# Optimization experiments

Hardware: AMD Instinct MI355X
Metric: run time of the kernel (lower is better)

The kernel has to match this reference:

```python
import jax, jax.numpy as jnp
import numpy as np

B, S, F, H = 64, 2048, 1024, 1024

def setup_inputs() -> dict:
    key = jax.random.key(0)
    ks = jax.random.split(key, 16)
    inp = {
        "input": jax.random.normal(ks[0], (B,), jnp.float32),
        "hidden": jax.random.normal(ks[1], (1, B, H), jnp.float32),
        "encoder_outputs": jax.random.normal(ks[2], (B, S, F), jnp.float32),
        "attention_mask": jax.random.randint(ks[3], (B, S), 0, 2, jnp.int32),
    }
    s = lambda n: 1.0 / np.sqrt(n)
    inp["attn_W"] = jax.random.uniform(ks[4], (1, F + H + 1), jnp.float32, -s(F+H+1), s(F+H+1))
    inp["attn_b"] = jax.random.uniform(ks[5], (1,), jnp.float32, -s(F+H+1), s(F+H+1))
    inp["combine_W"] = jax.random.uniform(ks[6], (H, F + 1), jnp.float32, -s(F+1), s(F+1))
    inp["combine_b"] = jax.random.uniform(ks[7], (H,), jnp.float32, -s(F+1), s(F+1))
    inp["W_ih"] = jax.random.uniform(ks[8], (3 * H, H), jnp.float32, -s(H), s(H))
    inp["W_hh"] = jax.random.uniform(ks[9], (3 * H, H), jnp.float32, -s(H), s(H))
    inp["b_ih"] = jax.random.uniform(ks[10], (3 * H,), jnp.float32, -s(H), s(H))
    inp["b_hh"] = jax.random.uniform(ks[11], (3 * H,), jnp.float32, -s(H), s(H))
    inp["out_W"] = jax.random.uniform(ks[12], (1, H), jnp.float32, -s(H), s(H))
    inp["out_b"] = jax.random.uniform(ks[13], (1,), jnp.float32, -s(H), s(H))
    return inp


def reference(input, hidden, encoder_outputs, attention_mask,
              attn_W, attn_b, combine_W, combine_b,
              W_ih, W_hh, b_ih, b_hh, out_W, out_b):
    # Dropout in eval mode (identity); faithful to deterministic inference.
    h = hidden[0]                                   # [B, H]
    # Additive attention score: Linear over cat(enc, h_expanded, input_expanded)
    # is split into three partial matmuls (same math, no [B,S,F+H+1] concat).
    w_e = attn_W[0, :F]                             # [F]
    w_h = attn_W[0, F:F + H]                        # [H]
    w_i = attn_W[0, -1]                             # scalar
    scores = (jnp.einsum('bsf,f->bs', encoder_outputs, w_e)
              + (h @ w_h)[:, None]
              + input[:, None] * w_i
              + attn_b[0])                          # [B, S]
    scores = jnp.where(attention_mask == 0, jnp.float32(-1e10), scores)
    attn_weights = jax.nn.softmax(scores, axis=1)   # [B, S]
    attn_applied = jnp.einsum('bs,bsf->bf', attn_weights, encoder_outputs)  # [B, F]

    x = jnp.concatenate([input[:, None], attn_applied], axis=1)  # [B, F+1]
    x = jax.nn.relu(x @ combine_W.T + combine_b)    # [B, H]

    # Single GRU step (PyTorch gate order: r, z, n)
    gi = x @ W_ih.T + b_ih                          # [B, 3H]
    gh = h @ W_hh.T + b_hh                          # [B, 3H]
    r = jax.nn.sigmoid(gi[:, :H] + gh[:, :H])
    z = jax.nn.sigmoid(gi[:, H:2 * H] + gh[:, H:2 * H])
    n = jnp.tanh(gi[:, 2 * H:] + r * gh[:, 2 * H:])
    h_new = (1.0 - z) * n + z * h                   # [B, H]

    out = jax.nn.relu(h_new) @ out_W.T + out_b      # [B, 1]
    return out[:, 0], h_new[None], attn_weights[:, :, None]
```

## Files before the change

### kernel.cpp

```cpp
#include <hip/hip_runtime.h>
#include <math.h>

#define BB 64
#define SS 2048
#define FF 1024
#define HH 1024
#define NCHUNK 32
#define KSPLIT 8
#define KCH 128

#define WS_PL    0
#define WS_XT    2048
#define WS_HT    (WS_XT+65536)
#define WS_X2T   (WS_HT+65536)
#define WS_EPART (WS_X2T+65536)
#define WS_GPART (WS_EPART+524288)
#define WS_PACC  (WS_GPART+3145728)

__device__ __forceinline__ float sigm(float x){ return 1.f/(1.f + __expf(-x)); }

__global__ __launch_bounds__(256) void kB(const float* __restrict__ enc,
                                          const int*   __restrict__ mask,
                                          const float* __restrict__ attn_W,
                                          const float* __restrict__ input,
                                          const float* __restrict__ hidden,
                                          const float* __restrict__ attn_b,
                                          float* __restrict__ scores_out,
                                          float* __restrict__ pacc,
                                          float* __restrict__ pl)
{
    const int tid  = threadIdx.x;
    const int lane = tid & 63;
    const int w    = tid >> 6;
    const int b    = blockIdx.x >> 5;
    const int c    = blockIdx.x & 31;
    const int s0   = c*64;

    const float4* we4 = (const float4*)attn_W;
    const float4 we0 = we4[lane], we1 = we4[64+lane], we2 = we4[128+lane], we3 = we4[192+lane];

    const float4* h4  = (const float4*)(hidden + (size_t)b*HH);
    const float4* wh4 = (const float4*)(attn_W + FF);
    float4 hv0 = h4[lane], hv1 = h4[64+lane], hv2 = h4[128+lane], hv3 = h4[192+lane];
    float4 wv0 = wh4[lane], wv1 = wh4[64+lane], wv2 = wh4[128+lane], wv3 = wh4[192+lane];
    float bp = hv0.x*wv0.x + hv0.y*wv0.y + hv0.z*wv0.z + hv0.w*wv0.w
             + hv1.x*wv1.x + hv1.y*wv1.y + hv1.z*wv1.z + hv1.w*wv1.w
             + hv2.x*wv2.x + hv2.y*wv2.y + hv2.z*wv2.z + hv2.w*wv2.w
             + hv3.x*wv3.x + hv3.y*wv3.y + hv3.z*wv3.z + hv3.w*wv3.w;
    #pragma unroll
    for (int off=32; off; off>>=1) bp += __shfl_xor(bp, off);
    const float bb = bp + input[b]*attn_W[FF+HH] + attn_b[0];

    int m = mask[b*SS + s0 + lane];
    unsigned long long v = __ballot(m != 0);
    int cnt = (int)__popcll(v);
    int share = (cnt + 3) >> 2;
    int start = w*share; if (start > cnt) start = cnt;
    int end = start + share; if (end > cnt) end = cnt;
    int mycount = end - start;

    unsigned long long vv = v;
    for (int i=0; i<start; ++i) vv &= vv - 1;

    const float4* encw = (const float4*)(enc + (size_t)(b*SS + s0)*FF);

    float l = 0.f;
    float4 a0 = make_float4(0,0,0,0), a1 = a0, a2 = a0, a3 = a0;
    float sc_keep = 0.f;
    unsigned long long written = 0ull;

    int npair = mycount >> 1;
    for (int p=0; p<npair; ++p){
        int rA = (int)__builtin_ctzll(vv); vv &= vv-1;
        int rB = (int)__builtin_ctzll(vv); vv &= vv-1;
        const float4* pA = encw + (size_t)rA*(FF/4);
        const float4* pB = encw + (size_t)rB*(FF/4);
        float4 e0 = pA[lane], e1 = pA[64+lane], e2 = pA[128+lane], e3 = pA[192+lane];
        float4 f0 = pB[lane], f1 = pB[64+lane], f2 = pB[128+lane], f3 = pB[192+lane];
        float da = (e0.x*we0.x + e0.y*we0.y + e0.z*we0.z + e0.w*we0.w)
                 + (e1.x*we1.x + e1.y*we1.y + e1.z*we1.z + e1.w*we1.w)
                 + (e2.x*we2.x + e2.y*we2.y + e2.z*we2.z + e2.w*we2.w)
                 + (e3.x*we3.x + e3.y*we3.y + e3.z*we3.z + e3.w*we3.w);
        float db = (f0.x*we0.x + f0.y*we0.y + f0.z*we0.z + f0.w*we0.w)
                 + (f1.x*we1.x + f1.y*we1.y + f1.z*we1.z + f1.w*we1.w)
                 + (f2.x*we2.x + f2.y*we2.y + f2.z*we2.z + f2.w*we2.w)
                 + (f3.x*we3.x + f3.y*we3.y + f3.z*we3.z + f3.w*we3.w);
        #pragma unroll
        for (int off=32; off; off>>=1){ da += __shfl_xor(da, off); db += __shfl_xor(db, off); }
        float scA = da + bb, scB = db + bb;
        float pAe = __expf(scA), pBe = __expf(scB);
        l += pAe + pBe;
        a0.x += pAe*e0.x + pBe*f0.x; a0.y += pAe*e0.y + pBe*f0.y; a0.z += pAe*e0.z + pBe*f0.z; a0.w += pAe*e0.w + pBe*f0.w;
        a1.x += pAe*e1.x + pBe*f1.x; a1.y += pAe*e1.y + pBe*f1.y; a1.z += pAe*e1.z + pBe*f1.z; a1.w += pAe*e1.w + pBe*f1.w;
        a2.x += pAe*e2.x + pBe*f2.x; a2.y += pAe*e2.y + pBe*f2.y; a2.z += pAe*e2.z + pBe*f2.z; a2.w += pAe*e2.w + pBe*f2.w;
        a3.x += pAe*e3.x + pBe*f3.x; a3.y += pAe*e3.y + pBe*f3.y; a3.z += pAe*e3.z + pBe*f3.z; a3.w += pAe*e3.w + pBe*f3.w;
        sc_keep = (lane == rA) ? scA : sc_keep;
        sc_keep = (lane == rB) ? scB : sc_keep;
        written |= (1ull << rA) | (1ull << rB);
    }
    if (mycount & 1){
        int rA = (int)__builtin_ctzll(vv);
        const float4* pA = encw + (size_t)rA*(FF/4);
        float4 e0 = pA[lane], e1 = pA[64+lane], e2 = pA[128+lane], e3 = pA[192+lane];
        float da = (e0.x*we0.x + e0.y*we0.y + e0.z*we0.z + e0.w*we0.w)
                 + (e1.x*we1.x + e1.y*we1.y + e1.z*we1.z + e1.w*we1.w)
                 + (e2.x*we2.x + e2.y*we2.y + e2.z*we2.z + e2.w*we2.w)
                 + (e3.x*we3.x + e3.y*we3.y + e3.z*we3.z + e3.w*we3.w);
        #pragma unroll
        for (int off=32; off; off>>=1) da += __shfl_xor(da, off);
        float scA = da + bb;
        float pAe = __expf(scA);
        l += pAe;
        a0.x += pAe*e0.x; a0.y += pAe*e0.y; a0.z += pAe*e0.z; a0.w += pAe*e0.w;
        a1.x += pAe*e1.x; a1.y += pAe*e1.y; a1.z += pAe*e1.z; a1.w += pAe*e1.w;
        a2.x += pAe*e2.x; a2.y += pAe*e2.y; a2.z += pAe*e2.z; a2.w += pAe*e2.w;
        a3.x += pAe*e3.x; a3.y += pAe*e3.y; a3.z += pAe*e3.z; a3.w += pAe*e3.w;
        sc_keep = (lane == rA) ? scA : sc_keep;
        written |= (1ull << rA);
    }
    if ((written >> lane) & 1ull) scores_out[b*SS + s0 + lane] = sc_keep;
    if (w == 0 && m == 0)         scores_out[b*SS + s0 + lane] = -1e10f;

    __shared__ float4 sacc[4][256];
    __shared__ float sl[4];
    if (lane==0) sl[w] = l;
    sacc[w][lane]     = a0;
    sacc[w][64+lane]  = a1;
    sacc[w][128+lane] = a2;
    sacc[w][192+lane] = a3;
    __syncthreads();
    float4 tot = sacc[0][tid];
    #pragma unroll
    for (int q=1;q<4;q++){ float4 u = sacc[q][tid]; tot.x+=u.x; tot.y+=u.y; tot.z+=u.z; tot.w+=u.w; }
    ((float4*)(pacc + (size_t)blockIdx.x*FF))[tid] = tot;
    if (tid==0) pl[blockIdx.x] = sl[0]+sl[1]+sl[2]+sl[3];
}

__global__ __launch_bounds__(256) void kC(const float* __restrict__ pacc,
                                          const float* __restrict__ pl,
                                          const float* __restrict__ hidden,
                                          const float* __restrict__ out_b,
                                          float* __restrict__ xT,
                                          float* __restrict__ wout,
                                          float* __restrict__ hT,
                                          float* __restrict__ out)
{
    int b = blockIdx.x >> 2, q = blockIdx.x & 3, tid = threadIdx.x;
    float L = 0.f;
    #pragma unroll
    for (int c=0;c<NCHUNK;c++) L += pl[b*NCHUNK+c];
    float invL = 1.f/L;

    int f = q*256 + tid;
    float a = 0.f;
    #pragma unroll
    for (int c=0;c<NCHUNK;c++) a += pacc[((size_t)(b*NCHUNK+c))*FF + f];
    xT[(size_t)f*BB + b] = a*invL;

    if (q == 0){
        for (int t = tid; t < SS; t += 256){
            int idx2 = b*SS + t;
            wout[idx2] = __expf(wout[idx2]) * invL;
        }
    } else if (q == 1){
        for (int k = tid; k < HH; k += 256) hT[(size_t)k*BB + b] = hidden[(size_t)b*HH + k];
    } else if (q == 2){
        if (tid == 0) out[b] = out_b[0];
    }
}

__global__ __launch_bounds__(256) void kE1(const float* __restrict__ xT,
                                           const float* __restrict__ cW,
                                           float* __restrict__ epart)
{
    __shared__ __align__(16) float Xl[KCH*64];
    __shared__ __align__(16) float Wl[16*KCH];
    int tid = threadIdx.x, lane = tid&63, w = tid>>6;
    int jb = blockIdx.x >> 3, kc = blockIdx.x & 7;
    int j0 = jb*16, k0 = kc*KCH;

    const float4* xs = (const float4*)(xT + (size_t)k0*BB);
    float4* xd = (float4*)Xl;
    #pragma unroll
    for (int r=tid; r<KCH*16; r+=256) xd[r] = xs[r];
    for (int idx=tid; idx<16*KCH; idx+=256){
        int row = idx>>7, kk = idx&127;
        Wl[idx] = cW[(size_t)(j0+row)*(FF+1) + 1 + k0 + kk];
    }
    __syncthreads();

    float acc[4] = {0.f,0.f,0.f,0.f};
    const float* wp = Wl + (w*4)*KCH;
    for (int kk=0; kk<KCH; kk+=4){
        float x0 = Xl[kk*64+lane], x1 = Xl[(kk+1)*64+lane];
        float x2 = Xl[(kk+2)*64+lane], x3 = Xl[(kk+3)*64+lane];
        #pragma unroll
        for (int jj=0;jj<4;jj++){
            float4 wv = *(const float4*)(wp + jj*KCH + kk);
            acc[jj] += x0*wv.x + x1*wv.y + x2*wv.z + x3*wv.w;
        }
    }
    #pragma unroll
    for (int jj=0;jj<4;jj++)
        epart[((size_t)kc*HH + j0 + w*4 + jj)*BB + lane] = acc[jj];
}

__global__ __launch_bounds__(256) void kE2(const float* __restrict__ epart,
                                           const float* __restrict__ input,
                                           const float* __restrict__ cW,
                                           const float* __restrict__ cb,
                                           float* __restrict__ x2T)
{
    int tid = threadIdx.x, lane = tid&63, w = tid>>6;
    int j = blockIdx.x*4 + w;
    float s = 0.f;
    #pragma unroll
    for (int kc=0;kc<KSPLIT;kc++) s += epart[((size_t)kc*HH + j)*BB + lane];
    s += input[lane]*cW[(size_t)j*(FF+1)] + cb[j];
    x2T[(size_t)j*BB + lane] = fmaxf(s, 0.f);
}

__global__ __launch_bounds__(256) void kF1(const float* __restrict__ x2T,
                                           const float* __restrict__ hT,
                                           const float* __restrict__ W_ih,
                                           const float* __restrict__ W_hh,
                                           float* __restrict__ gpart)
{
    __shared__ __align__(16) float Xl[KCH*64];
    __shared__ __align__(16) float Wl[16*KCH];
    int tid = threadIdx.x, lane = tid&63, w = tid>>6;
    int rb = blockIdx.x >> 3, kc = blockIdx.x & 7;
    int r0 = rb*16, k0 = kc*KCH;
    bool ih = (r0 < 3*HH);
    const float* X  = ih ? x2T : hT;
    const float* Wb = ih ? (W_ih + (size_t)r0*HH) : (W_hh + (size_t)(r0-3*HH)*HH);

    const float4* xs = (const float4*)(X + (size_t)k0*BB);
    float4* xd = (float4*)Xl;
    #pragma unroll
    for (int r=tid; r<KCH*16; r+=256) xd[r] = xs[r];
    float4* wd = (float4*)Wl;
    #pragma unroll
    for (int idx4=tid; idx4<16*KCH/4; idx4+=256){
        int row = idx4>>5, kq = idx4&31;
        wd[idx4] = *(const float4*)(Wb + (size_t)row*HH + k0 + kq*4);
    }
    __syncthreads();

    float acc[4] = {0.f,0.f,0.f,0.f};
    const float* wp = Wl + (w*4)*KCH;
    for (int kk=0; kk<KCH; kk+=4){
        float x0 = Xl[kk*64+lane], x1 = Xl[(kk+1)*64+lane];
        float x2 = Xl[(kk+2)*64+lane], x3 = Xl[(kk+3)*64+lane];
        #pragma unroll
        for (int jj=0;jj<4;jj++){
            float4 wv = *(const float4*)(wp + jj*KCH + kk);
            acc[jj] += x0*wv.x + x1*wv.y + x2*wv.z + x3*wv.w;
        }
    }
    #pragma unroll
    for (int jj=0;jj<4;jj++)
        gpart[((size_t)kc*6*HH + r0 + w*4 + jj)*BB + lane] = acc[jj];
}

__global__ __launch_bounds__(256) void kF2(const float* __restrict__ gpart,
                                           const float* __restrict__ b_ih,
                                           const float* __restrict__ b_hh,
                                           const float* __restrict__ hT,
                                           const float* __restrict__ out_W,
                                           float* __restrict__ hnew,
                                           float* __restrict__ out)
{
    int tid = threadIdx.x, lane = tid&63, w = tid>>6;
    int j = blockIdx.x*4 + w;
    float g[6];
    #pragma unroll
    for (int gi=0; gi<6; gi++){
        int row = (gi < 3) ? (gi*HH + j) : (3*HH + (gi-3)*HH + j);
        float s = 0.f;
        #pragma unroll
        for (int kc=0;kc<KSPLIT;kc++) s += gpart[((size_t)kc*6*HH + row)*BB + lane];
        g[gi] = s;
    }
    float r = sigm(g[0]+b_ih[j]        + g[3]+b_hh[j]);
    float z = sigm(g[1]+b_ih[HH+j]     + g[4]+b_hh[HH+j]);
    float n = tanhf(g[2]+b_ih[2*HH+j]  + r*(g[5]+b_hh[2*HH+j]));
    float hold = hT[(size_t)j*BB + lane];
    float hn = (1.f - z)*n + z*hold;
    hnew[(size_t)lane*HH + j] = hn;
    float pv = fmaxf(hn, 0.f) * out_W[j];
    __shared__ float red[4][64];
    red[w][lane] = pv;
    __syncthreads();
    if (w==0) atomicAdd(out + lane, red[0][lane]+red[1][lane]+red[2][lane]+red[3][lane]);
}

extern "C" void kernel_launch(void* const* d_in, const int* in_sizes, int n_in,
                              void* d_out, int out_size, void* d_ws, size_t ws_size,
                              hipStream_t stream) {
    const float* input     = (const float*)d_in[0];
    const float* hidden    = (const float*)d_in[1];
    const float* enc       = (const float*)d_in[2];
    const int*   mask      = (const int*)  d_in[3];
    const float* attn_W    = (const float*)d_in[4];
    const float* attn_b    = (const float*)d_in[5];
    const float* combine_W = (const float*)d_in[6];
    const float* combine_b = (const float*)d_in[7];
    const float* W_ih      = (const float*)d_in[8];
    const float* W_hh      = (const float*)d_in[9];
    const float* b_ih      = (const float*)d_in[10];
    const float* b_hh      = (const float*)d_in[11];
    const float* out_W     = (const float*)d_in[12];
    const float* out_b     = (const float*)d_in[13];

    float* out  = (float*)d_out;
    float* hnew = out + 64;
    float* attw = out + 64 + BB*HH;
    float* ws   = (float*)d_ws;

    kB <<<BB*NCHUNK, 256, 0, stream>>>(enc, mask, attn_W, input, hidden, attn_b,
                                       attw, ws+WS_PACC, ws+WS_PL);
    kC <<<256,  256, 0, stream>>>(ws+WS_PACC, ws+WS_PL, hidden, out_b,
                                  ws+WS_XT, attw, ws+WS_HT, out);
    kE1<<<512,  256, 0, stream>>>(ws+WS_XT, combine_W, ws+WS_EPART);
    kE2<<<256,  256, 0, stream>>>(ws+WS_EPART, input, combine_W, combine_b, ws+WS_X2T);
    kF1<<<3072, 256, 0, stream>>>(ws+WS_X2T, ws+WS_HT, W_ih, W_hh, ws+WS_GPART);
    kF2<<<256,  256, 0, stream>>>(ws+WS_GPART, b_ih, b_hh, ws+WS_HT, out_W, hnew, out);
}
```

Before: 102.5 us.

## Fold W_hh GEMV into attention kernel and drop hidden transpose staging

The h @ W_hh part of the GRU does not depend on attention, so it moves into extra blocks appended to the attention kernel's grid. It can then overlap with the memory-bound encoder pass instead of running after it in kF1. The hidden transpose in kC goes away; the new blocks read hidden row-wise and kF2 reads it directly. kE1 and kF1 also stop staging X in LDS and load x values from global into registers instead. The tradeoffs are more global traffic per block for x, and a heavier tail on the big attention launch.

```diff
diff --git a/kernel.cpp b/kernel.cpp
--- a/kernel.cpp
+++ b/kernel.cpp
@@ -11,27 +11,67 @@
 
 #define WS_PL    0
 #define WS_XT    2048
-#define WS_HT    (WS_XT+65536)
-#define WS_X2T   (WS_HT+65536)
+#define WS_X2T   (WS_XT+65536)
 #define WS_EPART (WS_X2T+65536)
 #define WS_GPART (WS_EPART+524288)
 #define WS_PACC  (WS_GPART+3145728)
 
 __device__ __forceinline__ float sigm(float x){ return 1.f/(1.f + __expf(-x)); }
 
-__global__ __launch_bounds__(256) void kB(const float* __restrict__ enc,
-                                          const int*   __restrict__ mask,
-                                          const float* __restrict__ attn_W,
-                                          const float* __restrict__ input,
-                                          const float* __restrict__ hidden,
-                                          const float* __restrict__ attn_b,
-                                          float* __restrict__ scores_out,
-                                          float* __restrict__ pacc,
-                                          float* __restrict__ pl)
-{
+__global__ __launch_bounds__(256) void kBH(const float* __restrict__ enc,
+                                           const int*   __restrict__ mask,
+                                           const float* __restrict__ attn_W,
+                                           const float* __restrict__ input,
+                                           const float* __restrict__ hidden,
+                                           const float* __restrict__ attn_b,
+                                           const float* __restrict__ W_hh,
+                                           float* __restrict__ scores_out,
+                                           float* __restrict__ pacc,
+                                           float* __restrict__ pl,
+                                           float* __restrict__ gpart)
+{
+    __shared__ __align__(16) char smem[16400];
     const int tid  = threadIdx.x;
     const int lane = tid & 63;
     const int w    = tid >> 6;
+
+    if (blockIdx.x >= 2048){
+        float* Wl = (float*)smem;
+        int idx = blockIdx.x - 2048;
+        int rb = idx >> 3, kc = idx & 7;
+        int r0 = rb*16, k0 = kc*KCH;
+        for (int t=tid; t<2048; t+=256){
+            int row = t>>7, kk = t&127;
+            Wl[t] = W_hh[(size_t)(r0+row)*HH + k0 + kk];
+        }
+        __syncthreads();
+        float acc[4] = {0.f,0.f,0.f,0.f};
+        const float* wp = Wl + (w*4)*KCH;
+        const float4* hr = (const float4*)(hidden + (size_t)lane*HH + k0);
+        for (int ks=0; ks<KCH; ks+=32){
+            float4 hv4[8];
+            #pragma unroll
+            for (int q=0;q<8;++q) hv4[q] = hr[(ks>>2) + q];
+            #pragma unroll
+            for (int q=0;q<8;++q){
+                int kk = ks + q*4;
+                float h0 = hv4[q].x, h1 = hv4[q].y, h2 = hv4[q].z, h3 = hv4[q].w;
+                #pragma unroll
+                for (int jj=0;jj<4;jj++){
+                    float4 wv = *(const float4*)(wp + jj*KCH + kk);
+                    acc[jj] += h0*wv.x + h1*wv.y + h2*wv.z + h3*wv.w;
+                }
+            }
+        }
+        #pragma unroll
+        for (int jj=0;jj<4;jj++)
+            gpart[((size_t)kc*6*HH + 3*HH + r0 + w*4 + jj)*BB + lane] = acc[jj];
+        return;
+    }
+
+    float4 (*sacc)[256] = (float4(*)[256])smem;
+    float* sl = (float*)(smem + 16384);
+
     const int b    = blockIdx.x >> 5;
     const int c    = blockIdx.x & 31;
     const int s0   = c*64;
@@ -121,8 +161,6 @@
     if ((written >> lane) & 1ull) scores_out[b*SS + s0 + lane] = sc_keep;
     if (w == 0 && m == 0)         scores_out[b*SS + s0 + lane] = -1e10f;
 
-    __shared__ float4 sacc[4][256];
-    __shared__ float sl[4];
     if (lane==0) sl[w] = l;
     sacc[w][lane]     = a0;
     sacc[w][64+lane]  = a1;
@@ -138,11 +176,9 @@
 
 __global__ __launch_bounds__(256) void kC(const float* __restrict__ pacc,
                                           const float* __restrict__ pl,
-                                          const float* __restrict__ hidden,
                                           const float* __restrict__ out_b,
                                           float* __restrict__ xT,
                                           float* __restrict__ wout,
-                                          float* __restrict__ hT,
                                           float* __restrict__ out)
 {
     int b = blockIdx.x >> 2, q = blockIdx.x & 3, tid = threadIdx.x;
@@ -163,8 +199,6 @@
             wout[idx2] = __expf(wout[idx2]) * invL;
         }
     } else if (q == 1){
-        for (int k = tid; k < HH; k += 256) hT[(size_t)k*BB + b] = hidden[(size_t)b*HH + k];
-    } else if (q == 2){
         if (tid == 0) out[b] = out_b[0];
     }
 }
@@ -173,16 +207,11 @@
                                            const float* __restrict__ cW,
                                            float* __restrict__ epart)
 {
-    __shared__ __align__(16) float Xl[KCH*64];
     __shared__ __align__(16) float Wl[16*KCH];
     int tid = threadIdx.x, lane = tid&63, w = tid>>6;
     int jb = blockIdx.x >> 3, kc = blockIdx.x & 7;
     int j0 = jb*16, k0 = kc*KCH;
 
-    const float4* xs = (const float4*)(xT + (size_t)k0*BB);
-    float4* xd = (float4*)Xl;
-    #pragma unroll
-    for (int r=tid; r<KCH*16; r+=256) xd[r] = xs[r];
     for (int idx=tid; idx<16*KCH; idx+=256){
         int row = idx>>7, kk = idx&127;
         Wl[idx] = cW[(size_t)(j0+row)*(FF+1) + 1 + k0 + kk];
@@ -191,13 +220,19 @@
 
     float acc[4] = {0.f,0.f,0.f,0.f};
     const float* wp = Wl + (w*4)*KCH;
-    for (int kk=0; kk<KCH; kk+=4){
-        float x0 = Xl[kk*64+lane], x1 = Xl[(kk+1)*64+lane];
-        float x2 = Xl[(kk+2)*64+lane], x3 = Xl[(kk+3)*64+lane];
-        #pragma unroll
-        for (int jj=0;jj<4;jj++){
-            float4 wv = *(const float4*)(wp + jj*KCH + kk);
-            acc[jj] += x0*wv.x + x1*wv.y + x2*wv.z + x3*wv.w;
+    for (int ks=0; ks<KCH; ks+=32){
+        float xv[32];
+        #pragma unroll
+        for (int i=0;i<32;++i) xv[i] = xT[(size_t)(k0+ks+i)*BB + lane];
+        #pragma unroll
+        for (int q=0;q<8;++q){
+            int kk = ks + q*4;
+            float x0 = xv[q*4+0], x1 = xv[q*4+1], x2 = xv[q*4+2], x3 = xv[q*4+3];
+            #pragma unroll
+            for (int jj=0;jj<4;jj++){
+                float4 wv = *(const float4*)(wp + jj*KCH + kk);
+                acc[jj] += x0*wv.x + x1*wv.y + x2*wv.z + x3*wv.w;
+            }
         }
     }
     #pragma unroll
@@ -221,41 +256,35 @@
 }
 
 __global__ __launch_bounds__(256) void kF1(const float* __restrict__ x2T,
-                                           const float* __restrict__ hT,
                                            const float* __restrict__ W_ih,
-                                           const float* __restrict__ W_hh,
                                            float* __restrict__ gpart)
 {
-    __shared__ __align__(16) float Xl[KCH*64];
     __shared__ __align__(16) float Wl[16*KCH];
     int tid = threadIdx.x, lane = tid&63, w = tid>>6;
     int rb = blockIdx.x >> 3, kc = blockIdx.x & 7;
     int r0 = rb*16, k0 = kc*KCH;
-    bool ih = (r0 < 3*HH);
-    const float* X  = ih ? x2T : hT;
-    const float* Wb = ih ? (W_ih + (size_t)r0*HH) : (W_hh + (size_t)(r0-3*HH)*HH);
-
-    const float4* xs = (const float4*)(X + (size_t)k0*BB);
-    float4* xd = (float4*)Xl;
-    #pragma unroll
-    for (int r=tid; r<KCH*16; r+=256) xd[r] = xs[r];
-    float4* wd = (float4*)Wl;
-    #pragma unroll
-    for (int idx4=tid; idx4<16*KCH/4; idx4+=256){
-        int row = idx4>>5, kq = idx4&31;
-        wd[idx4] = *(const float4*)(Wb + (size_t)row*HH + k0 + kq*4);
+
+    for (int t=tid; t<16*KCH; t+=256){
+        int row = t>>7, kk = t&127;
+        Wl[t] = W_ih[(size_t)(r0+row)*HH + k0 + kk];
     }
     __syncthreads();
 
     float acc[4] = {0.f,0.f,0.f,0.f};
     const float* wp = Wl + (w*4)*KCH;
-    for (int kk=0; kk<KCH; kk+=4){
-        float x0 = Xl[kk*64+lane], x1 = Xl[(kk+1)*64+lane];
-        float x2 = Xl[(kk+2)*64+lane], x3 = Xl[(kk+3)*64+lane];
-        #pragma unroll
-        for (int jj=0;jj<4;jj++){
-            float4 wv = *(const float4*)(wp + jj*KCH + kk);
-            acc[jj] += x0*wv.x + x1*wv.y + x2*wv.z + x3*wv.w;
+    for (int ks=0; ks<KCH; ks+=32){
+        float xv[32];
+        #pragma unroll
+        for (int i=0;i<32;++i) xv[i] = x2T[(size_t)(k0+ks+i)*BB + lane];
+        #pragma unroll
+        for (int q=0;q<8;++q){
+            int kk = ks + q*4;
+            float x0 = xv[q*4+0], x1 = xv[q*4+1], x2 = xv[q*4+2], x3 = xv[q*4+3];
+            #pragma unroll
+            for (int jj=0;jj<4;jj++){
+                float4 wv = *(const float4*)(wp + jj*KCH + kk);
+                acc[jj] += x0*wv.x + x1*wv.y + x2*wv.z + x3*wv.w;
+            }
         }
     }
     #pragma unroll
@@ -266,7 +295,7 @@
 __global__ __launch_bounds__(256) void kF2(const float* __restrict__ gpart,
                                            const float* __restrict__ b_ih,
                                            const float* __restrict__ b_hh,
-                                           const float* __restrict__ hT,
+                                           const float* __restrict__ hidden,
                                            const float* __restrict__ out_W,
                                            float* __restrict__ hnew,
                                            float* __restrict__ out)
@@ -285,7 +314,7 @@
     float r = sigm(g[0]+b_ih[j]        + g[3]+b_hh[j]);
     float z = sigm(g[1]+b_ih[HH+j]     + g[4]+b_hh[HH+j]);
     float n = tanhf(g[2]+b_ih[2*HH+j]  + r*(g[5]+b_hh[2*HH+j]));
-    float hold = hT[(size_t)j*BB + lane];
+    float hold = hidden[(size_t)lane*HH + j];
     float hn = (1.f - z)*n + z*hold;
     hnew[(size_t)lane*HH + j] = hn;
     float pv = fmaxf(hn, 0.f) * out_W[j];
@@ -318,12 +347,11 @@
     float* attw = out + 64 + BB*HH;
     float* ws   = (float*)d_ws;
 
-    kB <<<BB*NCHUNK, 256, 0, stream>>>(enc, mask, attn_W, input, hidden, attn_b,
-                                       attw, ws+WS_PACC, ws+WS_PL);
-    kC <<<256,  256, 0, stream>>>(ws+WS_PACC, ws+WS_PL, hidden, out_b,
-                                  ws+WS_XT, attw, ws+WS_HT, out);
+    kBH<<<BB*NCHUNK + 1536, 256, 0, stream>>>(enc, mask, attn_W, input, hidden, attn_b,
+                                              W_hh, attw, ws+WS_PACC, ws+WS_PL, ws+WS_GPART);
+    kC <<<256,  256, 0, stream>>>(ws+WS_PACC, ws+WS_PL, out_b, ws+WS_XT, attw, out);
     kE1<<<512,  256, 0, stream>>>(ws+WS_XT, combine_W, ws+WS_EPART);
     kE2<<<256,  256, 0, stream>>>(ws+WS_EPART, input, combine_W, combine_b, ws+WS_X2T);
-    kF1<<<3072, 256, 0, stream>>>(ws+WS_X2T, ws+WS_HT, W_ih, W_hh, ws+WS_GPART);
-    kF2<<<256,  256, 0, stream>>>(ws+WS_GPART, b_ih, b_hh, ws+WS_HT, out_W, hnew, out);
-}
+    kF1<<<1536, 256, 0, stream>>>(ws+WS_X2T, W_ih, ws+WS_GPART);
+    kF2<<<256,  256, 0, stream>>>(ws+WS_GPART, b_ih, b_hh, hidden, out_W, hnew, out);
+}
```

Result: slower. 118.5 us (+15.6%).
